# Kernel optimization log

Measured on AMD Instinct MI355X. Metric: run time of the kernel, lower is better.

Reference implementation:

```python
import jax, jax.numpy as jnp
import numpy as np

D_MODEL = 1024
N_HEADS = 16
D_K = D_MODEL // N_HEADS
MAX_LEN = 2048
B, T = 2, 2048


def setup_inputs() -> dict:
    key = jax.random.key(0)
    ks = jax.random.split(key, 10)
    s = 1.0 / np.sqrt(D_MODEL)
    inp = {
        "x": jax.random.normal(ks[0], (B, T, D_MODEL), dtype=jnp.float32),
        "WQ": jax.random.uniform(ks[1], (D_MODEL, D_MODEL), minval=-s, maxval=s, dtype=jnp.float32),
        "bQ": jax.random.uniform(ks[2], (D_MODEL,), minval=-s, maxval=s, dtype=jnp.float32),
        "WK": jax.random.uniform(ks[3], (D_MODEL, D_MODEL), minval=-s, maxval=s, dtype=jnp.float32),
        "bK": jax.random.uniform(ks[4], (D_MODEL,), minval=-s, maxval=s, dtype=jnp.float32),
        "WV": jax.random.uniform(ks[5], (D_MODEL, D_MODEL), minval=-s, maxval=s, dtype=jnp.float32),
        "bV": jax.random.uniform(ks[6], (D_MODEL,), minval=-s, maxval=s, dtype=jnp.float32),
        "WO": jax.random.uniform(ks[7], (D_MODEL, D_MODEL), minval=-s, maxval=s, dtype=jnp.float32),
        "bO": jax.random.uniform(ks[8], (D_MODEL,), minval=-s, maxval=s, dtype=jnp.float32),
        "rel_pos_table": jax.random.normal(ks[9], (2 * MAX_LEN - 1, N_HEADS), dtype=jnp.float32),
    }
    return inp


def reference(x, WQ, bQ, WK, bK, WV, bV, WO, bO, rel_pos_table):
    b, t, d = x.shape
    # torch Linear: y = x @ W^T + b
    q = (x @ WQ.T + bQ).reshape(b, t, N_HEADS, D_K).transpose(0, 2, 1, 3)  # [B,H,T,dk]
    k = (x @ WK.T + bK).reshape(b, t, N_HEADS, D_K).transpose(0, 2, 1, 3)
    v = (x @ WV.T + bV).reshape(b, t, N_HEADS, D_K).transpose(0, 2, 1, 3)

    scores = jnp.einsum("bhqd,bhkd->bhqk", q, k) / jnp.sqrt(jnp.float32(D_K))

    pos = jnp.arange(t)
    rel = pos[:, None] - pos[None, :] + (MAX_LEN - 1)
    rel = jnp.clip(rel, 0, 2 * MAX_LEN - 2)
    rel_bias = rel_pos_table[rel]                  # [T,T,H]
    scores = scores + rel_bias.transpose(2, 0, 1)[None]  # [1,H,T,T]

    causal = pos[None, :] <= pos[:, None]          # [T,T] lower-triangular
    scores = jnp.where(causal[None, None], scores, -jnp.inf)

    attn = jax.nn.softmax(scores, axis=-1)
    out = jnp.einsum("bhqk,bhkd->bhqd", attn, v)   # [B,H,T,dk]
    out = out.transpose(0, 2, 1, 3).reshape(b, t, d)
    return out @ WO.T + bO
```

## Files before the change

### kernel.cpp

```cpp
#include <hip/hip_runtime.h>
#include <hip/hip_bf16.h>

typedef __attribute__((ext_vector_type(8))) short bf16x8;
typedef __attribute__((ext_vector_type(4))) float f32x4;
typedef __attribute__((ext_vector_type(16))) float f32x16;

#define MFMA16(a, b, c) __builtin_amdgcn_mfma_f32_16x16x32_bf16(a, b, c, 0, 0, 0)
#define MFMA32(a, b, c) __builtin_amdgcn_mfma_f32_32x32x16_bf16(a, b, c, 0, 0, 0)

__device__ inline ushort f2b(float f) {
  union { float f; unsigned u; } v; v.f = f;
  unsigned u = v.u;
  u += 0x7fffu + ((u >> 16) & 1u);
  return (ushort)(u >> 16);
}

__device__ inline unsigned cvtpk(float lo, float hi) {
  unsigned r;
  asm("v_cvt_pk_bf16_f32 %0, %1, %2" : "=v"(r) : "v"(lo), "v"(hi));
  return r;
}

__device__ inline void plswap(unsigned& a, unsigned& b) {
  asm("v_permlane32_swap_b32 %0, %1" : "+v"(a), "+v"(b));
}

__global__ void cast_k(const float* __restrict__ in, ushort* __restrict__ out, int n) {
  int i = (blockIdx.x * blockDim.x + threadIdx.x) * 4;
  const int stride = gridDim.x * blockDim.x * 4;
  for (; i < n; i += stride) {
    float4 v = *reinterpret_cast<const float4*>(in + i);
    ushort4 o;
    o.x = f2b(v.x); o.y = f2b(v.y); o.z = f2b(v.z); o.w = f2b(v.w);
    *reinterpret_cast<ushort4*>(out + i) = o;
  }
}

__global__ void cast_w(const float* __restrict__ wq, const float* __restrict__ wk,
                       const float* __restrict__ wv, const float* __restrict__ wo,
                       ushort* __restrict__ wcat, ushort* __restrict__ wob) {
  const int i = (blockIdx.x * 256 + threadIdx.x) * 4;
  const int which = i >> 20, off = i & 1048575;
  const float* src = (which == 0) ? wq : (which == 1) ? wk : (which == 2) ? wv : wo;
  float4 v = *reinterpret_cast<const float4*>(src + off);
  ushort4 o;
  o.x = f2b(v.x); o.y = f2b(v.y); o.z = f2b(v.z); o.w = f2b(v.w);
  if (which < 3) *reinterpret_cast<ushort4*>(wcat + i) = o;
  else           *reinterpret_cast<ushort4*>(wob + off) = o;
}

__global__ void prep_rel(const float* __restrict__ relT, float* __restrict__ relvT) {
  const int t = blockIdx.x * 256 + threadIdx.x;
  if (t >= 16 * 4095) return;
  const int h = t / 4095, d = t - h * 4095;
  relvT[t] = relT[(size_t)d * 16 + h] * 1.4426950408889634f;
}

__global__ __launch_bounds__(256, 4)
void repack_kv(const ushort* __restrict__ Kg, const ushort* __restrict__ VTg,
               ushort* __restrict__ Kf, ushort* __restrict__ Vf) {
  const int blk = blockIdx.x;
  const int bh = blk >> 5, t64 = blk & 31;
  const int tid = threadIdx.x;
  const int w = tid >> 6, lane = tid & 63;
  const int li = lane & 31, hi = lane >> 5;
  const size_t dstbase = (size_t)blk * 4096 + lane * 8;
  const int half = w & 1;
  if (w < 2) {
#pragma unroll
    for (int c = 0; c < 4; ++c) {
      bf16x8 v = *reinterpret_cast<const bf16x8*>(
          Kg + ((size_t)(bh * 2048 + t64 * 64 + half * 32 + li)) * 64 + c * 16 + hi * 8);
      *reinterpret_cast<bf16x8*>(Kf + dstbase + (half * 4 + c) * 512) = v;
    }
  } else {
#pragma unroll
    for (int c = 0; c < 4; ++c) {
      bf16x8 v = *reinterpret_cast<const bf16x8*>(
          VTg + ((size_t)(bh * 64 + half * 32 + li)) * 2048 + t64 * 64 + c * 16 + hi * 8);
      *reinterpret_cast<bf16x8*>(Vf + dstbase + (half * 4 + c) * 512) = v;
    }
  }
}

template <int MODE>
__global__ __launch_bounds__(256, 3)
void gemm_bt(const ushort* __restrict__ A, const ushort* __restrict__ B,
             const float* __restrict__ b0, const float* __restrict__ b1,
             const float* __restrict__ b2,
             float* __restrict__ outF, ushort* __restrict__ Qg,
             ushort* __restrict__ Kg, ushort* __restrict__ VTg, int N) {
  __shared__ __align__(16) ushort As[128][32];
  __shared__ __align__(16) ushort Bs[128][32];
  const int tid = threadIdx.x;
  const int m0 = blockIdx.y * 128, n0 = blockIdx.x * 128;
  const int wid = tid >> 6, lane = tid & 63, g = lane >> 4, li = lane & 15;
  const int wr = (wid >> 1) * 64, wc = (wid & 1) * 64;
  const int srow = lane >> 2, scol = (lane & 3) * 8;
  const ushort* gA0 = A + (size_t)(m0 + wid * 32 + srow) * 1024 + scol;
  const ushort* gB0 = B + (size_t)(n0 + wid * 32 + srow) * 1024 + scol;
  ushort* lA0 = &As[wid * 32][0];
  ushort* lA1 = &As[wid * 32 + 16][0];
  ushort* lB0 = &Bs[wid * 32][0];
  ushort* lB1 = &Bs[wid * 32 + 16][0];
  f32x4 acc[4][4] = {};
  for (int k0 = 0; k0 < 1024; k0 += 32) {
    __builtin_amdgcn_global_load_lds((const __attribute__((address_space(1))) void*)(gA0 + k0),
                                     (__attribute__((address_space(3))) void*)lA0, 16, 0, 0);
    __builtin_amdgcn_global_load_lds((const __attribute__((address_space(1))) void*)(gA0 + 16 * 1024 + k0),
                                     (__attribute__((address_space(3))) void*)lA1, 16, 0, 0);
    __builtin_amdgcn_global_load_lds((const __attribute__((address_space(1))) void*)(gB0 + k0),
                                     (__attribute__((address_space(3))) void*)lB0, 16, 0, 0);
    __builtin_amdgcn_global_load_lds((const __attribute__((address_space(1))) void*)(gB0 + 16 * 1024 + k0),
                                     (__attribute__((address_space(3))) void*)lB1, 16, 0, 0);
    __syncthreads();
    bf16x8 af[4], bfm[4];
#pragma unroll
    for (int i = 0; i < 4; ++i) {
      af[i]  = *reinterpret_cast<const bf16x8*>(&As[wr + i * 16 + li][g * 8]);
      bfm[i] = *reinterpret_cast<const bf16x8*>(&Bs[wc + i * 16 + li][g * 8]);
    }
#pragma unroll
    for (int mi = 0; mi < 4; ++mi)
#pragma unroll
      for (int ni = 0; ni < 4; ++ni)
        acc[mi][ni] = MFMA16(af[mi], bfm[ni], acc[mi][ni]);
    __syncthreads();
  }
#pragma unroll
  for (int mi = 0; mi < 4; ++mi) {
#pragma unroll
    for (int ni = 0; ni < 4; ++ni) {
      const int col = n0 + wc + ni * 16 + li;
      if (MODE == 0) {
#pragma unroll
        for (int r = 0; r < 4; ++r) {
          const int row = m0 + wr + mi * 16 + 4 * g + r;
          outF[(size_t)row * N + col] = acc[mi][ni][r] + b0[col];
        }
      } else {
        const int which = col >> 10, c = col & 1023;
        const int hh = c >> 6, dk = c & 63;
        const float* bias = (which == 0) ? b0 : ((which == 1) ? b1 : b2);
        const float bcol = bias[c];
        const int row0 = m0 + wr + mi * 16 + 4 * g;
        const int bb = row0 >> 11, t0 = row0 & 2047;
        const size_t bhi = (size_t)(bb * 16 + hh);
        if (which == 2) {
          ushort4 o;
          o.x = f2b(acc[mi][ni][0] + bcol);
          o.y = f2b(acc[mi][ni][1] + bcol);
          o.z = f2b(acc[mi][ni][2] + bcol);
          o.w = f2b(acc[mi][ni][3] + bcol);
          *reinterpret_cast<ushort4*>(VTg + (bhi * 64 + dk) * 2048 + t0) = o;
        } else {
          ushort* dst = ((which == 0) ? Qg : Kg) + (bhi * 2048 + t0) * 64 + dk;
#pragma unroll
          for (int r = 0; r < 4; ++r)
            dst[(size_t)r * 64] = f2b(acc[mi][ni][r] + bcol);
        }
      }
    }
  }
}

__device__ __forceinline__ void attn_phase(
    const int qt, const int wid, const int lane, const int li, const int hi,
    const int h, const int bb,
    const ushort* __restrict__ Qb, const ushort* __restrict__ Kfb,
    const ushort* __restrict__ Vfb, const float* relv,
    float Obuf[3][64][33], float lbuf[3][64], ushort* __restrict__ Oa) {
  const int q = qt * 32 + li;
  bf16x8 qf[4];
#pragma unroll
  for (int c = 0; c < 4; ++c)
    qf[c] = *reinterpret_cast<const bf16x8*>(Qb + (size_t)q * 64 + c * 16 + hi * 8);
  f32x16 O[2] = {};
  float lacc[4] = {0.f, 0.f, 0.f, 0.f};
  const int nkt = (qt >> 1) + 1;
  const int nt = (wid < nkt) ? ((nkt - 1 - wid) >> 2) + 1 : 0;
  const int mask_kb = (nkt - 1) * 64;
  const float C1 = 0.18033688f;
  for (int i = 0; i < nt; ++i) {
    const int kb = wid * 64 + i * 256;
    const ushort* Kt = Kfb + (size_t)(kb >> 6) * 4096 + lane * 8;
    const ushort* Vt = Vfb + (size_t)(kb >> 6) * 4096 + lane * 8;
    bf16x8 Kr[8], Vr[8];
#pragma unroll
    for (int j = 0; j < 8; ++j)
      Kr[j] = *reinterpret_cast<const bf16x8*>(Kt + j * 512);
#pragma unroll
    for (int j = 0; j < 8; ++j)
      Vr[j] = *reinterpret_cast<const bf16x8*>(Vt + j * 512);
    __builtin_amdgcn_sched_barrier(0);
    f32x16 S0 = {}, S1 = {};
#pragma unroll
    for (int c = 0; c < 4; ++c) S0 = MFMA32(Kr[c], qf[c], S0);
#pragma unroll
    for (int c = 0; c < 4; ++c) S1 = MFMA32(Kr[4 + c], qf[c], S1);
    const int dqb = q - kb - 4 * hi;
    const float* rl = relv + (dqb - 63);
    if (kb != mask_kb) {
#pragma unroll
      for (int r = 0; r < 16; ++r) {
        const int off0 = (r & 3) + 8 * (r >> 2);
        const float p0 = __builtin_amdgcn_exp2f(fmaf(S0[r], C1, rl[63 - off0]));
        const float p1 = __builtin_amdgcn_exp2f(fmaf(S1[r], C1, rl[31 - off0]));
        S0[r] = p0; S1[r] = p1;
        lacc[r & 3] += p0 + p1;
      }
    } else {
#pragma unroll
      for (int r = 0; r < 16; ++r) {
        const int off0 = (r & 3) + 8 * (r >> 2);
        const int d0 = dqb - off0, d1 = d0 - 32;
        float p0 = __builtin_amdgcn_exp2f(fmaf(S0[r], C1, relv[d0 & 2047]));
        float p1 = __builtin_amdgcn_exp2f(fmaf(S1[r], C1, relv[d1 & 2047]));
        p0 = (d0 >= 0) ? p0 : 0.f;
        p1 = (d1 >= 0) ? p1 : 0.f;
        S0[r] = p0; S1[r] = p1;
        lacc[r & 3] += p0 + p1;
      }
    }
    unsigned U0[4][2], U1[4][2];
#pragma unroll
    for (int rg = 0; rg < 4; ++rg) {
      U0[rg][0] = cvtpk(S0[4 * rg + 0], S0[4 * rg + 1]);
      U0[rg][1] = cvtpk(S0[4 * rg + 2], S0[4 * rg + 3]);
      U1[rg][0] = cvtpk(S1[4 * rg + 0], S1[4 * rg + 1]);
      U1[rg][1] = cvtpk(S1[4 * rg + 2], S1[4 * rg + 3]);
    }
#pragma unroll
    for (int c = 0; c < 4; ++c) {
      const int c0 = c & 1;
      unsigned x0 = (c < 2) ? U0[2 * c0][0] : U1[2 * c0][0];
      unsigned y0 = (c < 2) ? U0[2 * c0 + 1][0] : U1[2 * c0 + 1][0];
      unsigned x1 = (c < 2) ? U0[2 * c0][1] : U1[2 * c0][1];
      unsigned y1 = (c < 2) ? U0[2 * c0 + 1][1] : U1[2 * c0 + 1][1];
      plswap(x0, y0);
      plswap(x1, y1);
      union { unsigned u[4]; bf16x8 v; } P;
      P.u[0] = x0; P.u[1] = x1; P.u[2] = y0; P.u[3] = y1;
#pragma unroll
      for (int db = 0; db < 2; ++db)
        O[db] = MFMA32(Vr[db * 4 + c], P.v, O[db]);
    }
  }
  __syncthreads();
  if (wid) {
    float* ob = &Obuf[wid - 1][lane][0];
#pragma unroll
    for (int db = 0; db < 2; ++db)
#pragma unroll
      for (int r = 0; r < 16; ++r)
        ob[db * 16 + r] = O[db][r];
    lbuf[wid - 1][lane] = lacc[0] + lacc[1] + lacc[2] + lacc[3];
  }
  __syncthreads();
  if (wid == 0) {
    float lh = lacc[0] + lacc[1] + lacc[2] + lacc[3];
#pragma unroll
    for (int w = 0; w < 3; ++w) {
      lh += lbuf[w][lane];
      const float* ob = &Obuf[w][lane][0];
#pragma unroll
      for (int db = 0; db < 2; ++db)
#pragma unroll
        for (int r = 0; r < 16; ++r)
          O[db][r] += ob[db * 16 + r];
    }
    unsigned xa = __float_as_uint(lh), xb2 = xa;
    plswap(xa, xb2);
    const float linv = 1.f / (__uint_as_float(xa) + __uint_as_float(xb2));
    ushort* orow = Oa + ((size_t)(bb * 2048 + q)) * 1024 + h * 64;
#pragma unroll
    for (int db = 0; db < 2; ++db)
#pragma unroll
      for (int rg = 0; rg < 4; ++rg) {
        ushort4 o;
        o.x = f2b(O[db][4 * rg + 0] * linv);
        o.y = f2b(O[db][4 * rg + 1] * linv);
        o.z = f2b(O[db][4 * rg + 2] * linv);
        o.w = f2b(O[db][4 * rg + 3] * linv);
        *reinterpret_cast<ushort4*>(orow + db * 32 + 8 * rg + 4 * hi) = o;
      }
  }
}

__global__ __launch_bounds__(256, 2)
void attn_k(const ushort* __restrict__ Qg, const ushort* __restrict__ Kf,
            const ushort* __restrict__ Vf, const float* __restrict__ relvT,
            ushort* __restrict__ Oa) {
  __shared__ float relv[2048];
  __shared__ float Obuf[3][64][33];
  __shared__ float lbuf[3][64];
  const int f = blockIdx.x;
  const int bh = (f & 7) * 4 + (f >> 8);
  const int qp = (f >> 3) & 31;
  const int h = bh & 15, bb = bh >> 4;
  {
    const float* src = relvT + h * 4095 + 2047;
    for (int i = threadIdx.x; i < 2048; i += 256) relv[i] = src[i];
  }
  __syncthreads();
  const int wid = threadIdx.x >> 6, lane = threadIdx.x & 63;
  const int li = lane & 31, hi = lane >> 5;
  const ushort* Qb  = Qg + (size_t)bh * (2048 * 64);
  const ushort* Kfb = Kf + (size_t)bh * (32 * 4096);
  const ushort* Vfb = Vf + (size_t)bh * (32 * 4096);
  attn_phase(qp,      wid, lane, li, hi, h, bb, Qb, Kfb, Vfb, relv, Obuf, lbuf, Oa);
  attn_phase(63 - qp, wid, lane, li, hi, h, bb, Qb, Kfb, Vfb, relv, Obuf, lbuf, Oa);
}

extern "C" void kernel_launch(void* const* d_in, const int* in_sizes, int n_in,
                              void* d_out, int out_size, void* d_ws, size_t ws_size,
                              hipStream_t stream) {
  const float* x    = (const float*)d_in[0];
  const float* WQ   = (const float*)d_in[1];
  const float* bQ   = (const float*)d_in[2];
  const float* WK   = (const float*)d_in[3];
  const float* bK   = (const float*)d_in[4];
  const float* WV   = (const float*)d_in[5];
  const float* bV   = (const float*)d_in[6];
  const float* WO   = (const float*)d_in[7];
  const float* bO   = (const float*)d_in[8];
  const float* relT = (const float*)d_in[9];
  float* out = (float*)d_out;

  if (ws_size < (size_t)48 * 1024 * 1024) return;

  char* ws = (char*)d_ws;
  const size_t MB = 1024 * 1024;
  ushort* xb    = (ushort*)(ws);
  ushort* Kf    = (ushort*)(ws);
  ushort* Wcat  = (ushort*)(ws + 8 * MB);
  float*  relvT = (float*)(ws + 8 * MB);
  ushort* WOb   = (ushort*)(ws + 14 * MB);
  ushort* Qg    = (ushort*)(ws + 16 * MB);
  ushort* Kg    = (ushort*)(ws + 24 * MB);
  ushort* VTg   = (ushort*)(ws + 32 * MB);
  ushort* Oa    = (ushort*)(ws + 32 * MB);
  ushort* Vf    = (ushort*)(ws + 40 * MB);

  cast_k<<<1024, 256, 0, stream>>>(x, xb, 4096 * 1024);
  cast_w<<<4096, 256, 0, stream>>>(WQ, WK, WV, WO, Wcat, WOb);

  gemm_bt<1><<<dim3(24, 32), 256, 0, stream>>>(xb, Wcat, bQ, bK, bV,
                                               nullptr, Qg, Kg, VTg, 3072);
  prep_rel<<<256, 256, 0, stream>>>(relT, relvT);
  repack_kv<<<1024, 256, 0, stream>>>(Kg, VTg, Kf, Vf);
  attn_k<<<1024, 256, 0, stream>>>(Qg, Kf, Vf, relvT, Oa);
  gemm_bt<0><<<dim3(8, 32), 256, 0, stream>>>(Oa, WOb, bO, nullptr, nullptr,
                                              out, nullptr, nullptr, nullptr, 1024);
}
```

Before: 122.8 us.

## Fuse K/V repack into QKV GEMM epilogue, widen GEMM K-tile, vectorize rel bias

The QKV projection GEMM now writes K and V straight into the fragment-friendly layouts the attention kernel reads, so the separate repack_kv kernel and its extra global round trip go away. The GEMM K-step grows from 32 to 64, which halves the number of barrier-separated iterations but doubles LDS per block. Relative-position bias is also precomputed as float4 windows with an XOR swizzle in LDS, so attention fetches four bias values per load instead of four scalar loads. The epilogue stores for K/V become scattered short writes, and the larger LDS footprint may lower occupancy.

```diff
diff --git a/kernel.cpp b/kernel.cpp
--- a/kernel.cpp
+++ b/kernel.cpp
@@ -49,38 +49,16 @@
   else           *reinterpret_cast<ushort4*>(wob + off) = o;
 }
 
-__global__ void prep_rel(const float* __restrict__ relT, float* __restrict__ relvT) {
+__global__ void prep_f4(const float* __restrict__ relT, float4* __restrict__ relF4) {
   const int t = blockIdx.x * 256 + threadIdx.x;
-  if (t >= 16 * 4095) return;
-  const int h = t / 4095, d = t - h * 4095;
-  relvT[t] = relT[(size_t)d * 16 + h] * 1.4426950408889634f;
-}
-
-__global__ __launch_bounds__(256, 4)
-void repack_kv(const ushort* __restrict__ Kg, const ushort* __restrict__ VTg,
-               ushort* __restrict__ Kf, ushort* __restrict__ Vf) {
-  const int blk = blockIdx.x;
-  const int bh = blk >> 5, t64 = blk & 31;
-  const int tid = threadIdx.x;
-  const int w = tid >> 6, lane = tid & 63;
-  const int li = lane & 31, hi = lane >> 5;
-  const size_t dstbase = (size_t)blk * 4096 + lane * 8;
-  const int half = w & 1;
-  if (w < 2) {
-#pragma unroll
-    for (int c = 0; c < 4; ++c) {
-      bf16x8 v = *reinterpret_cast<const bf16x8*>(
-          Kg + ((size_t)(bh * 2048 + t64 * 64 + half * 32 + li)) * 64 + c * 16 + hi * 8);
-      *reinterpret_cast<bf16x8*>(Kf + dstbase + (half * 4 + c) * 512) = v;
-    }
-  } else {
-#pragma unroll
-    for (int c = 0; c < 4; ++c) {
-      bf16x8 v = *reinterpret_cast<const bf16x8*>(
-          VTg + ((size_t)(bh * 64 + half * 32 + li)) * 2048 + t64 * 64 + c * 16 + hi * 8);
-      *reinterpret_cast<bf16x8*>(Vf + dstbase + (half * 4 + c) * 512) = v;
-    }
-  }
+  const int h = t >> 11, i = t & 2047;
+  const float C = 1.4426950408889634f;
+  float4 v;
+  v.x = relT[(size_t)(i + 2047) * 16 + h] * C;
+  v.y = (i >= 1) ? relT[(size_t)(i + 2046) * 16 + h] * C : 0.f;
+  v.z = (i >= 2) ? relT[(size_t)(i + 2045) * 16 + h] * C : 0.f;
+  v.w = (i >= 3) ? relT[(size_t)(i + 2044) * 16 + h] * C : 0.f;
+  relF4[(size_t)h * 2048 + i] = v;
 }
 
 template <int MODE>
@@ -89,42 +67,41 @@
              const float* __restrict__ b0, const float* __restrict__ b1,
              const float* __restrict__ b2,
              float* __restrict__ outF, ushort* __restrict__ Qg,
-             ushort* __restrict__ Kg, ushort* __restrict__ VTg, int N) {
-  __shared__ __align__(16) ushort As[128][32];
-  __shared__ __align__(16) ushort Bs[128][32];
+             ushort* __restrict__ Kf, ushort* __restrict__ Vf, int N) {
+  __shared__ __align__(16) ushort As[128][64];
+  __shared__ __align__(16) ushort Bs[128][64];
   const int tid = threadIdx.x;
   const int m0 = blockIdx.y * 128, n0 = blockIdx.x * 128;
   const int wid = tid >> 6, lane = tid & 63, g = lane >> 4, li = lane & 15;
   const int wr = (wid >> 1) * 64, wc = (wid & 1) * 64;
-  const int srow = lane >> 2, scol = (lane & 3) * 8;
-  const ushort* gA0 = A + (size_t)(m0 + wid * 32 + srow) * 1024 + scol;
-  const ushort* gB0 = B + (size_t)(n0 + wid * 32 + srow) * 1024 + scol;
-  ushort* lA0 = &As[wid * 32][0];
-  ushort* lA1 = &As[wid * 32 + 16][0];
-  ushort* lB0 = &Bs[wid * 32][0];
-  ushort* lB1 = &Bs[wid * 32 + 16][0];
+  const int srow0 = (lane >> 3), scol = (lane & 7) * 8;
   f32x4 acc[4][4] = {};
-  for (int k0 = 0; k0 < 1024; k0 += 32) {
-    __builtin_amdgcn_global_load_lds((const __attribute__((address_space(1))) void*)(gA0 + k0),
-                                     (__attribute__((address_space(3))) void*)lA0, 16, 0, 0);
-    __builtin_amdgcn_global_load_lds((const __attribute__((address_space(1))) void*)(gA0 + 16 * 1024 + k0),
-                                     (__attribute__((address_space(3))) void*)lA1, 16, 0, 0);
-    __builtin_amdgcn_global_load_lds((const __attribute__((address_space(1))) void*)(gB0 + k0),
-                                     (__attribute__((address_space(3))) void*)lB0, 16, 0, 0);
-    __builtin_amdgcn_global_load_lds((const __attribute__((address_space(1))) void*)(gB0 + 16 * 1024 + k0),
-                                     (__attribute__((address_space(3))) void*)lB1, 16, 0, 0);
+  for (int k0 = 0; k0 < 1024; k0 += 64) {
+#pragma unroll
+    for (int it = 0; it < 4; ++it) {
+      const int rb = (wid * 4 + it) * 8;
+      __builtin_amdgcn_global_load_lds(
+          (const __attribute__((address_space(1))) void*)(A + (size_t)(m0 + rb + srow0) * 1024 + k0 + scol),
+          (__attribute__((address_space(3))) void*)(&As[0][0] + (wid * 4 + it) * 512), 16, 0, 0);
+      __builtin_amdgcn_global_load_lds(
+          (const __attribute__((address_space(1))) void*)(B + (size_t)(n0 + rb + srow0) * 1024 + k0 + scol),
+          (__attribute__((address_space(3))) void*)(&Bs[0][0] + (wid * 4 + it) * 512), 16, 0, 0);
+    }
     __syncthreads();
-    bf16x8 af[4], bfm[4];
-#pragma unroll
-    for (int i = 0; i < 4; ++i) {
-      af[i]  = *reinterpret_cast<const bf16x8*>(&As[wr + i * 16 + li][g * 8]);
-      bfm[i] = *reinterpret_cast<const bf16x8*>(&Bs[wc + i * 16 + li][g * 8]);
-    }
-#pragma unroll
-    for (int mi = 0; mi < 4; ++mi)
-#pragma unroll
-      for (int ni = 0; ni < 4; ++ni)
-        acc[mi][ni] = MFMA16(af[mi], bfm[ni], acc[mi][ni]);
+#pragma unroll
+    for (int kk = 0; kk < 64; kk += 32) {
+      bf16x8 af[4], bfm[4];
+#pragma unroll
+      for (int i = 0; i < 4; ++i) {
+        af[i]  = *reinterpret_cast<const bf16x8*>(&As[wr + i * 16 + li][kk + g * 8]);
+        bfm[i] = *reinterpret_cast<const bf16x8*>(&Bs[wc + i * 16 + li][kk + g * 8]);
+      }
+#pragma unroll
+      for (int mi = 0; mi < 4; ++mi)
+#pragma unroll
+        for (int ni = 0; ni < 4; ++ni)
+          acc[mi][ni] = MFMA16(af[mi], bfm[ni], acc[mi][ni]);
+    }
     __syncthreads();
   }
 #pragma unroll
@@ -145,19 +122,28 @@
         const float bcol = bias[c];
         const int row0 = m0 + wr + mi * 16 + 4 * g;
         const int bb = row0 >> 11, t0 = row0 & 2047;
-        const size_t bhi = (size_t)(bb * 16 + hh);
-        if (which == 2) {
+        const int bhi = bb * 16 + hh;
+        if (which == 0) {
+          ushort* dst = Qg + ((size_t)bhi * 2048 + t0) * 64 + dk;
+#pragma unroll
+          for (int r = 0; r < 4; ++r)
+            dst[(size_t)r * 64] = f2b(acc[mi][ni][r] + bcol);
+        } else if (which == 1) {
+          const size_t cb = ((size_t)((bhi * 32 + (t0 >> 6)) * 8 + ((t0 >> 5) & 1) * 4 + (dk >> 4))) * 512
+                            + ((dk >> 3) & 1) * 256 + (dk & 7);
+          ushort* dst = Kf + cb + (t0 & 31) * 8;
+#pragma unroll
+          for (int r = 0; r < 4; ++r)
+            dst[r * 8] = f2b(acc[mi][ni][r] + bcol);
+        } else {
+          const size_t cb = ((size_t)((bhi * 32 + (t0 >> 6)) * 8 + (dk >> 5) * 4 + ((t0 >> 4) & 3))) * 512
+                            + (dk & 31) * 8 + ((t0 >> 3) & 1) * 256 + (t0 & 7);
           ushort4 o;
           o.x = f2b(acc[mi][ni][0] + bcol);
           o.y = f2b(acc[mi][ni][1] + bcol);
           o.z = f2b(acc[mi][ni][2] + bcol);
           o.w = f2b(acc[mi][ni][3] + bcol);
-          *reinterpret_cast<ushort4*>(VTg + (bhi * 64 + dk) * 2048 + t0) = o;
-        } else {
-          ushort* dst = ((which == 0) ? Qg : Kg) + (bhi * 2048 + t0) * 64 + dk;
-#pragma unroll
-          for (int r = 0; r < 4; ++r)
-            dst[(size_t)r * 64] = f2b(acc[mi][ni][r] + bcol);
+          *reinterpret_cast<ushort4*>(Vf + cb) = o;
         }
       }
     }
@@ -168,7 +154,7 @@
     const int qt, const int wid, const int lane, const int li, const int hi,
     const int h, const int bb,
     const ushort* __restrict__ Qb, const ushort* __restrict__ Kfb,
-    const ushort* __restrict__ Vfb, const float* relv,
+    const ushort* __restrict__ Vfb, const float4* relv4,
     float Obuf[3][64][33], float lbuf[3][64], ushort* __restrict__ Oa) {
   const int q = qt * 32 + li;
   bf16x8 qf[4];
@@ -199,27 +185,42 @@
 #pragma unroll
     for (int c = 0; c < 4; ++c) S1 = MFMA32(Kr[4 + c], qf[c], S1);
     const int dqb = q - kb - 4 * hi;
-    const float* rl = relv + (dqb - 63);
     if (kb != mask_kb) {
 #pragma unroll
-      for (int r = 0; r < 16; ++r) {
-        const int off0 = (r & 3) + 8 * (r >> 2);
-        const float p0 = __builtin_amdgcn_exp2f(fmaf(S0[r], C1, rl[63 - off0]));
-        const float p1 = __builtin_amdgcn_exp2f(fmaf(S1[r], C1, rl[31 - off0]));
-        S0[r] = p0; S1[r] = p1;
-        lacc[r & 3] += p0 + p1;
+      for (int rg = 0; rg < 4; ++rg) {
+        const int i0 = dqb - 8 * rg, i1 = i0 - 32;
+        const float4 bq0 = relv4[i0 ^ ((i0 >> 3) & 3)];
+        const float4 bq1 = relv4[i1 ^ ((i1 >> 3) & 3)];
+        const float b0e[4] = {bq0.x, bq0.y, bq0.z, bq0.w};
+        const float b1e[4] = {bq1.x, bq1.y, bq1.z, bq1.w};
+#pragma unroll
+        for (int j = 0; j < 4; ++j) {
+          const int r = 4 * rg + j;
+          const float p0 = __builtin_amdgcn_exp2f(fmaf(S0[r], C1, b0e[j]));
+          const float p1 = __builtin_amdgcn_exp2f(fmaf(S1[r], C1, b1e[j]));
+          S0[r] = p0; S1[r] = p1;
+          lacc[j] += p0 + p1;
+        }
       }
     } else {
 #pragma unroll
-      for (int r = 0; r < 16; ++r) {
-        const int off0 = (r & 3) + 8 * (r >> 2);
-        const int d0 = dqb - off0, d1 = d0 - 32;
-        float p0 = __builtin_amdgcn_exp2f(fmaf(S0[r], C1, relv[d0 & 2047]));
-        float p1 = __builtin_amdgcn_exp2f(fmaf(S1[r], C1, relv[d1 & 2047]));
-        p0 = (d0 >= 0) ? p0 : 0.f;
-        p1 = (d1 >= 0) ? p1 : 0.f;
-        S0[r] = p0; S1[r] = p1;
-        lacc[r & 3] += p0 + p1;
+      for (int rg = 0; rg < 4; ++rg) {
+        const int d0b = dqb - 8 * rg, d1b = d0b - 32;
+        const int i0 = d0b & 2047, i1 = d1b & 2047;
+        const float4 bq0 = relv4[i0 ^ ((i0 >> 3) & 3)];
+        const float4 bq1 = relv4[i1 ^ ((i1 >> 3) & 3)];
+        const float b0e[4] = {bq0.x, bq0.y, bq0.z, bq0.w};
+        const float b1e[4] = {bq1.x, bq1.y, bq1.z, bq1.w};
+#pragma unroll
+        for (int j = 0; j < 4; ++j) {
+          const int r = 4 * rg + j;
+          float p0 = __builtin_amdgcn_exp2f(fmaf(S0[r], C1, b0e[j]));
+          float p1 = __builtin_amdgcn_exp2f(fmaf(S1[r], C1, b1e[j]));
+          p0 = (d0b - j >= 0) ? p0 : 0.f;
+          p1 = (d1b - j >= 0) ? p1 : 0.f;
+          S0[r] = p0; S1[r] = p1;
+          lacc[j] += p0 + p1;
+        }
       }
     }
     unsigned U0[4][2], U1[4][2];
@@ -289,9 +290,9 @@
 
 __global__ __launch_bounds__(256, 2)
 void attn_k(const ushort* __restrict__ Qg, const ushort* __restrict__ Kf,
-            const ushort* __restrict__ Vf, const float* __restrict__ relvT,
+            const ushort* __restrict__ Vf, const float4* __restrict__ relF4,
             ushort* __restrict__ Oa) {
-  __shared__ float relv[2048];
+  __shared__ __align__(16) float4 relv4[2048];
   __shared__ float Obuf[3][64][33];
   __shared__ float lbuf[3][64];
   const int f = blockIdx.x;
@@ -299,8 +300,9 @@
   const int qp = (f >> 3) & 31;
   const int h = bh & 15, bb = bh >> 4;
   {
-    const float* src = relvT + h * 4095 + 2047;
-    for (int i = threadIdx.x; i < 2048; i += 256) relv[i] = src[i];
+    const float4* src = relF4 + (size_t)h * 2048;
+    for (int i = threadIdx.x; i < 2048; i += 256)
+      relv4[i ^ ((i >> 3) & 3)] = src[i];
   }
   __syncthreads();
   const int wid = threadIdx.x >> 6, lane = threadIdx.x & 63;
@@ -308,8 +310,8 @@
   const ushort* Qb  = Qg + (size_t)bh * (2048 * 64);
   const ushort* Kfb = Kf + (size_t)bh * (32 * 4096);
   const ushort* Vfb = Vf + (size_t)bh * (32 * 4096);
-  attn_phase(qp,      wid, lane, li, hi, h, bb, Qb, Kfb, Vfb, relv, Obuf, lbuf, Oa);
-  attn_phase(63 - qp, wid, lane, li, hi, h, bb, Qb, Kfb, Vfb, relv, Obuf, lbuf, Oa);
+  attn_phase(qp,      wid, lane, li, hi, h, bb, Qb, Kfb, Vfb, relv4, Obuf, lbuf, Oa);
+  attn_phase(63 - qp, wid, lane, li, hi, h, bb, Qb, Kfb, Vfb, relv4, Obuf, lbuf, Oa);
 }
 
 extern "C" void kernel_launch(void* const* d_in, const int* in_sizes, int n_in,
@@ -332,24 +334,21 @@
   char* ws = (char*)d_ws;
   const size_t MB = 1024 * 1024;
   ushort* xb    = (ushort*)(ws);
-  ushort* Kf    = (ushort*)(ws);
+  float4* relF4 = (float4*)(ws);
   ushort* Wcat  = (ushort*)(ws + 8 * MB);
-  float*  relvT = (float*)(ws + 8 * MB);
   ushort* WOb   = (ushort*)(ws + 14 * MB);
   ushort* Qg    = (ushort*)(ws + 16 * MB);
-  ushort* Kg    = (ushort*)(ws + 24 * MB);
-  ushort* VTg   = (ushort*)(ws + 32 * MB);
-  ushort* Oa    = (ushort*)(ws + 32 * MB);
-  ushort* Vf    = (ushort*)(ws + 40 * MB);
+  ushort* Kf    = (ushort*)(ws + 24 * MB);
+  ushort* Vf    = (ushort*)(ws + 32 * MB);
+  ushort* Oa    = (ushort*)(ws + 40 * MB);
 
   cast_k<<<1024, 256, 0, stream>>>(x, xb, 4096 * 1024);
   cast_w<<<4096, 256, 0, stream>>>(WQ, WK, WV, WO, Wcat, WOb);
 
   gemm_bt<1><<<dim3(24, 32), 256, 0, stream>>>(xb, Wcat, bQ, bK, bV,
-                                               nullptr, Qg, Kg, VTg, 3072);
-  prep_rel<<<256, 256, 0, stream>>>(relT, relvT);
-  repack_kv<<<1024, 256, 0, stream>>>(Kg, VTg, Kf, Vf);
-  attn_k<<<1024, 256, 0, stream>>>(Qg, Kf, Vf, relvT, Oa);
+                                               nullptr, Qg, Kf, Vf, 3072);
+  prep_f4<<<128, 256, 0, stream>>>(relT, relF4);
+  attn_k<<<1024, 256, 0, stream>>>(Qg, Kf, Vf, relF4, Oa);
   gemm_bt<0><<<dim3(8, 32), 256, 0, stream>>>(Oa, WOb, bO, nullptr, nullptr,
                                               out, nullptr, nullptr, nullptr, 1024);
 }
```

Result: faster. 114.9 us (-6.4%).
